# Kernel optimization log

Hardware: AMD Instinct MI355X
Metric: run time of the kernel (lower is better)

The kernel has to match this reference:

```python
import jax, jax.numpy as jnp
import numpy as np

B, R, F, H, DIM = 256, 64, 2048, 512, 512

def setup_inputs() -> dict:
    key = jax.random.key(0)
    ks = jax.random.split(key, 8)
    s = lambda n: 1.0 / np.sqrt(n)
    return {
        "features": jax.random.normal(ks[0], (B, R, F), jnp.float32),
        "prev": jax.random.normal(ks[1], (B, H), jnp.float32),
        "W_w": jax.random.normal(ks[2], (F, DIM), jnp.float32) * s(F),
        "W_b": jnp.zeros((DIM,), jnp.float32),
        "W2_w": jax.random.normal(ks[3], (H, DIM), jnp.float32) * s(H),
        "W2_b": jnp.zeros((DIM,), jnp.float32),
        "W3_w": jax.random.normal(ks[4], (DIM, 1), jnp.float32) * s(DIM),
        "W3_b": jnp.zeros((1,), jnp.float32),
    }

def reference(features, prev, W_w, W_b, W2_w, W2_b, W3_w, W3_b):
    # prev: [B,H] -> [B,1,DIM]
    p = (prev @ W2_w + W2_b)[:, None, :]
    # features: [B,R,F] -> [B,R,DIM]
    c = jnp.einsum('brf,fd->brd', features, W_w) + W_b
    c = jnp.tanh(c + p)
    score = jnp.einsum('brd,do->bro', c, W3_w) + W3_b  # [B,R,1]
    aw = jax.nn.softmax(score, axis=1)
    q = jnp.sum(aw * features, axis=1)  # [B,F]
    return q
```

## Files before the change

kernel.cpp:

```cpp
#include <hip/hip_runtime.h>
#include <hip/hip_bf16.h>


#define B_ 256
#define R_ 64
#define F_ 2048
#define H_ 512
#define DIM_ 512

typedef short bf16x8 __attribute__((ext_vector_type(8)));
typedef float f32x4 __attribute__((ext_vector_type(4)));

__device__ __forceinline__ ushort f2bf(float x) {
  __hip_bfloat16 h = __float2bfloat16(x);
  return __builtin_bit_cast(ushort, h);
}

__device__ __forceinline__ uint2 pack4(float4 x) {
  uint2 r;
  r.x = (uint)f2bf(x.x) | ((uint)f2bf(x.y) << 16);
  r.y = (uint)f2bf(x.z) | ((uint)f2bf(x.w) << 16);
  return r;
}

__global__ __launch_bounds__(256) void setup_k(const float* __restrict__ Ww,
                                               ushort* __restrict__ wpack,
                                               const float* __restrict__ prev,
                                               const float* __restrict__ W2w,
                                               const float* __restrict__ W2b,
                                               const float* __restrict__ Wb,
                                               float* __restrict__ pprime) {
  __shared__ float lprev[8][H_];
  if (blockIdx.x < 4096) {
    int idx = blockIdx.x * 256 + threadIdx.x;
    float v = Ww[idx];
    int k = idx >> 9;
    int d = idx & 511;
    int kt = k >> 5, kr = k & 31;
    int g = kr >> 3, i = kr & 7;
    int ctg = d >> 4, c = d & 15;
    size_t dst = ((size_t)((kt * 32 + ctg) * 64 + g * 16 + c)) * 8 + (size_t)i;
    wpack[dst] = f2bf(v);
    return;
  }
  int pb = blockIdx.x - 4096;
  int bg = pb >> 3;
  int d0 = (pb & 7) * 64;
  int t = threadIdx.x;
  const float4* src = reinterpret_cast<const float4*>(prev + (size_t)bg * 8 * H_);
  float4* dst = reinterpret_cast<float4*>(&lprev[0][0]);
  for (int i = t; i < 8 * H_ / 4; i += 256) dst[i] = src[i];
  __syncthreads();
  int d = d0 + (t & 63);
  int bq = t >> 6;
  float a0 = 0.f, a1 = 0.f;
  #pragma unroll 8
  for (int h = 0; h < H_; ++h) {
    float wv = W2w[h * DIM_ + d];
    a0 += lprev[bq][h] * wv;
    a1 += lprev[bq + 4][h] * wv;
  }
  float bias = W2b[d] + Wb[d];
  pprime[(size_t)(bg * 8 + bq) * DIM_ + d] = a0 + bias;
  pprime[(size_t)(bg * 8 + bq + 4) * DIM_ + d] = a1 + bias;
}

__device__ __forceinline__ float fast_tanh(float x) {
  float e = __expf(2.f * x);
  return 1.f - 2.f / (e + 1.f);
}

__global__ __launch_bounds__(512, 4) void score_k(const float* __restrict__ feat,
                                                  const ushort* __restrict__ wpack,
                                                  const float* __restrict__ pprime,
                                                  const float* __restrict__ W3,
                                                  float* __restrict__ sp) {
  int slice = blockIdx.x >> 8;
  int b = blockIdx.x & 255;
  int t = threadIdx.x;
  int wid = t >> 6;
  int l = t & 63;
  int l15 = l & 15, g = l >> 4;
  const float* featB = feat + (size_t)b * R_ * F_;

  __shared__ uint4 frg[2][512];
  __shared__ float lds_part[8][R_];

  f32x4 acc[4][2];
  #pragma unroll
  for (int rt = 0; rt < 4; ++rt)
    #pragma unroll
    for (int ct = 0; ct < 2; ++ct)
      acc[rt][ct] = (f32x4){0.f, 0.f, 0.f, 0.f};

  int r0 = t >> 4;
  int c4 = t & 15;
  const float* ga0 = featB + (size_t)r0 * F_ + (size_t)(c4 * 4);
  const float* ga1 = featB + (size_t)(r0 + 32) * F_ + (size_t)(c4 * 4);
  int kcw = c4 >> 1, half = c4 & 1;
  int wi0 = kcw * 64 + (r0 ^ kcw);
  int wi1 = kcw * 64 + ((r0 + 32) ^ kcw);

  const ushort* wp = wpack + (size_t)(slice * 16 + wid * 2) * 512 + (size_t)l * 8;

#define LOADB(dst, kt) do {                                          \
    const ushort* wpk_ = wp + (size_t)(kt) * 32768;                  \
    dst[0][0] = *reinterpret_cast<const uint4*>(wpk_);               \
    dst[0][1] = *reinterpret_cast<const uint4*>(wpk_ + 512);         \
    dst[1][0] = *reinterpret_cast<const uint4*>(wpk_ + 16384);       \
    dst[1][1] = *reinterpret_cast<const uint4*>(wpk_ + 16384 + 512); \
  } while (0)

#define CVTW(fb, ASET) do {                                          \
    uint2* d0_ = reinterpret_cast<uint2*>(&frg[fb][wi0]);            \
    d0_[half] = pack4(ASET[0]);                                      \
    uint2* d1_ = reinterpret_cast<uint2*>(&frg[fb][wi1]);            \
    d1_[half] = pack4(ASET[1]);                                      \
  } while (0)

#define MFMA8(AF, BSET, s_) do {                                     \
    _Pragma("unroll")                                                \
    for (int ct_ = 0; ct_ < 2; ++ct_) {                              \
      bf16x8 bv_ = __builtin_bit_cast(bf16x8, BSET[s_][ct_]);        \
      _Pragma("unroll")                                              \
      for (int rt_ = 0; rt_ < 4; ++rt_)                              \
        acc[rt_][ct_] = __builtin_amdgcn_mfma_f32_16x16x32_bf16(     \
            __builtin_bit_cast(bf16x8, AF[rt_]), bv_, acc[rt_][ct_], 0, 0, 0); \
    }                                                                \
  } while (0)

#define FENCE() asm volatile("" ::: "memory")
#define BAR() do { FENCE(); __builtin_amdgcn_s_barrier(); FENCE(); } while (0)
#define LGKM0() do {                                                 \
    asm volatile("s_waitcnt lgkmcnt(0)" ::: "memory");               \
    __builtin_amdgcn_sched_barrier(0);                               \
  } while (0)

#define REGION(kt, aCvt, aFill, bUse, bFill) do {                    \
    uint4 af0_[4], af1_[4];                                          \
    _Pragma("unroll")                                                \
    for (int rt_ = 0; rt_ < 4; ++rt_)                                \
      af0_[rt_] = frg[(kt) & 1][g * 64 + ((rt_ * 16 + l15) ^ g)];    \
    if ((kt) < 30) {                                                 \
      aFill[0] = *reinterpret_cast<const float4*>(ga0 + ((kt) + 2) * 64); \
      aFill[1] = *reinterpret_cast<const float4*>(ga1 + ((kt) + 2) * 64); \
    }                                                                \
    if ((kt) < 31) LOADB(bFill, (kt) + 1);                           \
    BAR();                                                           \
    LGKM0();                                                         \
    __builtin_amdgcn_s_setprio(1);                                   \
    MFMA8(af0_, bUse, 0);                                            \
    __builtin_amdgcn_s_setprio(0);                                   \
    BAR();                                                           \
    _Pragma("unroll")                                                \
    for (int rt_ = 0; rt_ < 4; ++rt_) {                              \
      int kc_ = 4 + g;                                               \
      af1_[rt_] = frg[(kt) & 1][kc_ * 64 + ((rt_ * 16 + l15) ^ kc_)]; \
    }                                                                \
    if ((kt) < 31) CVTW(((kt) + 1) & 1, aCvt);                       \
    BAR();                                                           \
    LGKM0();                                                         \
    __builtin_amdgcn_s_setprio(1);                                   \
    MFMA8(af1_, bUse, 1);                                            \
    __builtin_amdgcn_s_setprio(0);                                   \
    BAR();                                                           \
  } while (0)

  float4 aS0[2], aS1[2];
  uint4 b0[2][2], b1[2][2];

  aS0[0] = *reinterpret_cast<const float4*>(ga0);
  aS0[1] = *reinterpret_cast<const float4*>(ga1);
  LOADB(b0, 0);
  CVTW(0, aS0);
  aS1[0] = *reinterpret_cast<const float4*>(ga0 + 64);
  aS1[1] = *reinterpret_cast<const float4*>(ga1 + 64);
  LGKM0();
  BAR();

  for (int kt = 0; kt < 32; kt += 2) {
    REGION(kt, aS1, aS0, b0, b1);
    REGION(kt + 1, aS0, aS1, b1, b0);
  }

#undef LOADB
#undef CVTW
#undef MFMA8
#undef REGION
#undef BAR
#undef LGKM0
#undef FENCE

  float pp[2], w3v[2];
  #pragma unroll
  for (int ct = 0; ct < 2; ++ct) {
    int col = slice * 256 + wid * 32 + ct * 16 + l15;
    pp[ct] = pprime[b * DIM_ + col];
    w3v[ct] = W3[col];
  }
  #pragma unroll
  for (int rt = 0; rt < 4; ++rt) {
    #pragma unroll
    for (int j = 0; j < 4; ++j) {
      float v = fast_tanh(acc[rt][0][j] + pp[0]) * w3v[0]
              + fast_tanh(acc[rt][1][j] + pp[1]) * w3v[1];
      v += __shfl_xor(v, 1);
      v += __shfl_xor(v, 2);
      v += __shfl_xor(v, 4);
      v += __shfl_xor(v, 8);
      if (l15 == 0) lds_part[wid][rt * 16 + g * 4 + j] = v;
    }
  }
  __syncthreads();

  if (t < R_) {
    float s = 0.f;
    #pragma unroll
    for (int w = 0; w < 8; ++w) s += lds_part[w][t];
    sp[((size_t)b * 2 + slice) * R_ + t] = s;
  }
}

__global__ __launch_bounds__(256) void wsum_k(const float* __restrict__ feat,
                                              const float* __restrict__ sp,
                                              float* __restrict__ out) {
  int b = blockIdx.x >> 2;
  int f0 = (blockIdx.x & 3) * 512;
  int t = threadIdx.x;
  __shared__ float lds_aw[R_];

  if (t < R_) {
    float s = sp[((size_t)b * 2 + 0) * R_ + t] + sp[((size_t)b * 2 + 1) * R_ + t];
    float m = s;
    #pragma unroll
    for (int off = 32; off >= 1; off >>= 1) m = fmaxf(m, __shfl_xor(m, off));
    float e = __expf(s - m);
    float su = e;
    #pragma unroll
    for (int off = 32; off >= 1; off >>= 1) su += __shfl_xor(su, off);
    lds_aw[t] = e / su;
  }
  __syncthreads();

  const float* fp = feat + (size_t)b * R_ * F_ + f0 + t * 2;
  float qx = 0.f, qy = 0.f;
  #pragma unroll 8
  for (int r = 0; r < R_; ++r) {
    float a = lds_aw[r];
    float2 v = *reinterpret_cast<const float2*>(fp + (size_t)r * F_);
    qx += a * v.x;
    qy += a * v.y;
  }
  *reinterpret_cast<float2*>(out + (size_t)b * F_ + f0 + t * 2) = (float2){qx, qy};
}

extern "C" void kernel_launch(void* const* d_in, const int* in_sizes, int n_in,
                              void* d_out, int out_size, void* d_ws, size_t ws_size,
                              hipStream_t stream) {
  const float* feat = (const float*)d_in[0];
  const float* prev = (const float*)d_in[1];
  const float* Ww   = (const float*)d_in[2];
  const float* Wb   = (const float*)d_in[3];
  const float* W2w  = (const float*)d_in[4];
  const float* W2b  = (const float*)d_in[5];
  const float* W3w  = (const float*)d_in[6];
  float* out = (float*)d_out;

  ushort* wpack  = (ushort*)d_ws;
  float*  pprime = (float*)((char*)d_ws + (size_t)F_ * DIM_ * 2);
  float*  sp     = (float*)((char*)d_ws + (size_t)F_ * DIM_ * 2
                                        + (size_t)B_ * DIM_ * 4);

  setup_k<<<4096 + 256, 256, 0, stream>>>(Ww, wpack, prev, W2w, W2b, Wb, pprime);
  score_k<<<B_ * 2, 512, 0, stream>>>(feat, wpack, pprime, W3w, sp);
  wsum_k<<<B_ * 4, 256, 0, stream>>>(feat, sp, out);
}
```

Measured before the change: 117.7 us.

## Split score kernel into single-wave blocks over 64-column DIM slices

Restructures the score kernel so each 64-thread block handles one batch and 64 DIM columns. Each wave loads and converts the full feature tile itself, with no block barriers and a single LDS buffer. Partial scores for 8 slices are summed in the softmax kernel. This removes barrier synchronisation and raises block count. In exchange, each batch's features are read and converted to bf16 eight times instead of twice, and register pressure is higher.

After: 199.7 us. 69.7% more time.

```diff
diff --git a/kernel.cpp b/kernel.cpp
--- a/kernel.cpp
+++ b/kernel.cpp
@@ -70,131 +70,112 @@
   return 1.f - 2.f / (e + 1.f);
 }
 
-__global__ __launch_bounds__(512, 4) void score_k(const float* __restrict__ feat,
-                                                  const ushort* __restrict__ wpack,
-                                                  const float* __restrict__ pprime,
-                                                  const float* __restrict__ W3,
-                                                  float* __restrict__ sp) {
+__global__ __launch_bounds__(64, 2) void score_k(const float* __restrict__ feat,
+                                                 const ushort* __restrict__ wpack,
+                                                 const float* __restrict__ pprime,
+                                                 const float* __restrict__ W3,
+                                                 float* __restrict__ sp) {
   int slice = blockIdx.x >> 8;
   int b = blockIdx.x & 255;
-  int t = threadIdx.x;
-  int wid = t >> 6;
-  int l = t & 63;
+  int l = threadIdx.x;
   int l15 = l & 15, g = l >> 4;
   const float* featB = feat + (size_t)b * R_ * F_;
 
-  __shared__ uint4 frg[2][512];
-  __shared__ float lds_part[8][R_];
-
-  f32x4 acc[4][2];
+  __shared__ uint4 frg[512];
+  __shared__ float sc[R_];
+
+  f32x4 acc[4][4];
   #pragma unroll
   for (int rt = 0; rt < 4; ++rt)
     #pragma unroll
-    for (int ct = 0; ct < 2; ++ct)
+    for (int ct = 0; ct < 4; ++ct)
       acc[rt][ct] = (f32x4){0.f, 0.f, 0.f, 0.f};
 
-  int r0 = t >> 4;
-  int c4 = t & 15;
-  const float* ga0 = featB + (size_t)r0 * F_ + (size_t)(c4 * 4);
-  const float* ga1 = featB + (size_t)(r0 + 32) * F_ + (size_t)(c4 * 4);
+  int c4 = l & 15, r4 = l >> 4;
   int kcw = c4 >> 1, half = c4 & 1;
-  int wi0 = kcw * 64 + (r0 ^ kcw);
-  int wi1 = kcw * 64 + ((r0 + 32) ^ kcw);
-
-  const ushort* wp = wpack + (size_t)(slice * 16 + wid * 2) * 512 + (size_t)l * 8;
+  const float* aptr = featB + (size_t)r4 * F_ + (size_t)(c4 * 4);
+  float4 rA[16];
+
+  const ushort* wp = wpack + (size_t)(slice * 4) * 512 + (size_t)l * 8;
+
+#define LOADA(kt) do {                                               \
+    _Pragma("unroll")                                                \
+    for (int j_ = 0; j_ < 16; ++j_)                                  \
+      rA[j_] = *reinterpret_cast<const float4*>(                     \
+          aptr + (size_t)(j_ * 4) * F_ + (size_t)(kt) * 64);         \
+  } while (0)
+
+#define CVTW() do {                                                  \
+    _Pragma("unroll")                                                \
+    for (int j_ = 0; j_ < 16; ++j_) {                                \
+      int row_ = r4 + 4 * j_;                                        \
+      uint2* d_ = reinterpret_cast<uint2*>(&frg[kcw * 64 + (row_ ^ kcw)]); \
+      d_[half] = pack4(rA[j_]);                                      \
+    }                                                                \
+  } while (0)
 
 #define LOADB(dst, kt) do {                                          \
     const ushort* wpk_ = wp + (size_t)(kt) * 32768;                  \
-    dst[0][0] = *reinterpret_cast<const uint4*>(wpk_);               \
-    dst[0][1] = *reinterpret_cast<const uint4*>(wpk_ + 512);         \
-    dst[1][0] = *reinterpret_cast<const uint4*>(wpk_ + 16384);       \
-    dst[1][1] = *reinterpret_cast<const uint4*>(wpk_ + 16384 + 512); \
-  } while (0)
-
-#define CVTW(fb, ASET) do {                                          \
-    uint2* d0_ = reinterpret_cast<uint2*>(&frg[fb][wi0]);            \
-    d0_[half] = pack4(ASET[0]);                                      \
-    uint2* d1_ = reinterpret_cast<uint2*>(&frg[fb][wi1]);            \
-    d1_[half] = pack4(ASET[1]);                                      \
-  } while (0)
-
-#define MFMA8(AF, BSET, s_) do {                                     \
-    _Pragma("unroll")                                                \
-    for (int ct_ = 0; ct_ < 2; ++ct_) {                              \
-      bf16x8 bv_ = __builtin_bit_cast(bf16x8, BSET[s_][ct_]);        \
+    _Pragma("unroll")                                                \
+    for (int s_ = 0; s_ < 2; ++s_)                                   \
+      _Pragma("unroll")                                              \
+      for (int ct_ = 0; ct_ < 4; ++ct_)                              \
+        dst[s_ * 4 + ct_] = *reinterpret_cast<const uint4*>(         \
+            wpk_ + s_ * 16384 + ct_ * 512);                          \
+  } while (0)
+
+#define STEP(k, BUSE, BNXT) do {                                     \
+    if ((k) < 31) LOADB(BNXT, (k) + 1);                              \
+    uint4 af0_[4], af1_[4];                                          \
+    _Pragma("unroll")                                                \
+    for (int rt_ = 0; rt_ < 4; ++rt_)                                \
+      af0_[rt_] = frg[g * 64 + ((rt_ * 16 + l15) ^ g)];              \
+    _Pragma("unroll")                                                \
+    for (int rt_ = 0; rt_ < 4; ++rt_) {                              \
+      int kc_ = 4 + g;                                               \
+      af1_[rt_] = frg[kc_ * 64 + ((rt_ * 16 + l15) ^ kc_)];          \
+    }                                                                \
+    if ((k) < 31) CVTW();             \
+    if ((k) < 30) LOADA((k) + 2);                                    \
+    _Pragma("unroll")                                                \
+    for (int ct_ = 0; ct_ < 4; ++ct_) {                              \
+      bf16x8 bv_ = __builtin_bit_cast(bf16x8, BUSE[ct_]);            \
       _Pragma("unroll")                                              \
       for (int rt_ = 0; rt_ < 4; ++rt_)                              \
         acc[rt_][ct_] = __builtin_amdgcn_mfma_f32_16x16x32_bf16(     \
-            __builtin_bit_cast(bf16x8, AF[rt_]), bv_, acc[rt_][ct_], 0, 0, 0); \
-    }                                                                \
-  } while (0)
-
-#define FENCE() asm volatile("" ::: "memory")
-#define BAR() do { FENCE(); __builtin_amdgcn_s_barrier(); FENCE(); } while (0)
-#define LGKM0() do {                                                 \
-    asm volatile("s_waitcnt lgkmcnt(0)" ::: "memory");               \
-    __builtin_amdgcn_sched_barrier(0);                               \
-  } while (0)
-
-#define REGION(kt, aCvt, aFill, bUse, bFill) do {                    \
-    uint4 af0_[4], af1_[4];                                          \
-    _Pragma("unroll")                                                \
-    for (int rt_ = 0; rt_ < 4; ++rt_)                                \
-      af0_[rt_] = frg[(kt) & 1][g * 64 + ((rt_ * 16 + l15) ^ g)];    \
-    if ((kt) < 30) {                                                 \
-      aFill[0] = *reinterpret_cast<const float4*>(ga0 + ((kt) + 2) * 64); \
-      aFill[1] = *reinterpret_cast<const float4*>(ga1 + ((kt) + 2) * 64); \
-    }                                                                \
-    if ((kt) < 31) LOADB(bFill, (kt) + 1);                           \
-    BAR();                                                           \
-    LGKM0();                                                         \
-    __builtin_amdgcn_s_setprio(1);                                   \
-    MFMA8(af0_, bUse, 0);                                            \
-    __builtin_amdgcn_s_setprio(0);                                   \
-    BAR();                                                           \
-    _Pragma("unroll")                                                \
-    for (int rt_ = 0; rt_ < 4; ++rt_) {                              \
-      int kc_ = 4 + g;                                               \
-      af1_[rt_] = frg[(kt) & 1][kc_ * 64 + ((rt_ * 16 + l15) ^ kc_)]; \
-    }                                                                \
-    if ((kt) < 31) CVTW(((kt) + 1) & 1, aCvt);                       \
-    BAR();                                                           \
-    LGKM0();                                                         \
-    __builtin_amdgcn_s_setprio(1);                                   \
-    MFMA8(af1_, bUse, 1);                                            \
-    __builtin_amdgcn_s_setprio(0);                                   \
-    BAR();                                                           \
-  } while (0)
-
-  float4 aS0[2], aS1[2];
-  uint4 b0[2][2], b1[2][2];
-
-  aS0[0] = *reinterpret_cast<const float4*>(ga0);
-  aS0[1] = *reinterpret_cast<const float4*>(ga1);
-  LOADB(b0, 0);
-  CVTW(0, aS0);
-  aS1[0] = *reinterpret_cast<const float4*>(ga0 + 64);
-  aS1[1] = *reinterpret_cast<const float4*>(ga1 + 64);
-  LGKM0();
-  BAR();
-
-  for (int kt = 0; kt < 32; kt += 2) {
-    REGION(kt, aS1, aS0, b0, b1);
-    REGION(kt + 1, aS0, aS1, b1, b0);
-  }
-
+            __builtin_bit_cast(bf16x8, af0_[rt_]), bv_, acc[rt_][ct_], 0, 0, 0); \
+    }                                                                \
+    _Pragma("unroll")                                                \
+    for (int ct_ = 0; ct_ < 4; ++ct_) {                              \
+      bf16x8 bv_ = __builtin_bit_cast(bf16x8, BUSE[4 + ct_]);        \
+      _Pragma("unroll")                                              \
+      for (int rt_ = 0; rt_ < 4; ++rt_)                              \
+        acc[rt_][ct_] = __builtin_amdgcn_mfma_f32_16x16x32_bf16(     \
+            __builtin_bit_cast(bf16x8, af1_[rt_]), bv_, acc[rt_][ct_], 0, 0, 0); \
+    }                                                                \
+  } while (0)
+
+  uint4 bE[8], bO[8];
+  LOADA(0);
+  LOADB(bE, 0);
+  CVTW();
+  LOADA(1);
+
+  #pragma unroll 1
+  for (int k = 0; k < 32; k += 2) {
+    STEP(k, bE, bO);
+    STEP(k + 1, bO, bE);
+  }
+
+#undef LOADA
+#undef CVTW
 #undef LOADB
-#undef CVTW
-#undef MFMA8
-#undef REGION
-#undef BAR
-#undef LGKM0
-#undef FENCE
-
-  float pp[2], w3v[2];
+#undef STEP
+
+  float pp[4], w3v[4];
   #pragma unroll
-  for (int ct = 0; ct < 2; ++ct) {
-    int col = slice * 256 + wid * 32 + ct * 16 + l15;
+  for (int ct = 0; ct < 4; ++ct) {
+    int col = slice * 64 + ct * 16 + l15;
     pp[ct] = pprime[b * DIM_ + col];
     w3v[ct] = W3[col];
   }
@@ -203,22 +184,17 @@
     #pragma unroll
     for (int j = 0; j < 4; ++j) {
       float v = fast_tanh(acc[rt][0][j] + pp[0]) * w3v[0]
-              + fast_tanh(acc[rt][1][j] + pp[1]) * w3v[1];
+              + fast_tanh(acc[rt][1][j] + pp[1]) * w3v[1]
+              + fast_tanh(acc[rt][2][j] + pp[2]) * w3v[2]
+              + fast_tanh(acc[rt][3][j] + pp[3]) * w3v[3];
       v += __shfl_xor(v, 1);
       v += __shfl_xor(v, 2);
       v += __shfl_xor(v, 4);
       v += __shfl_xor(v, 8);
-      if (l15 == 0) lds_part[wid][rt * 16 + g * 4 + j] = v;
+      if (l15 == 0) sc[rt * 16 + g * 4 + j] = v;
     }
   }
-  __syncthreads();
-
-  if (t < R_) {
-    float s = 0.f;
-    #pragma unroll
-    for (int w = 0; w < 8; ++w) s += lds_part[w][t];
-    sp[((size_t)b * 2 + slice) * R_ + t] = s;
-  }
+  sp[((size_t)b * 8 + slice) * R_ + l] = sc[l];
 }
 
 __global__ __launch_bounds__(256) void wsum_k(const float* __restrict__ feat,
@@ -230,7 +206,9 @@
   __shared__ float lds_aw[R_];
 
   if (t < R_) {
-    float s = sp[((size_t)b * 2 + 0) * R_ + t] + sp[((size_t)b * 2 + 1) * R_ + t];
+    float s = 0.f;
+    #pragma unroll
+    for (int i = 0; i < 8; ++i) s += sp[((size_t)b * 8 + i) * R_ + t];
     float m = s;
     #pragma unroll
     for (int off = 32; off >= 1; off >>= 1) m = fmaxf(m, __shfl_xor(m, off));
@@ -272,6 +250,6 @@
                                         + (size_t)B_ * DIM_ * 4);
 
   setup_k<<<4096 + 256, 256, 0, stream>>>(Ww, wpack, prev, W2w, W2b, Wb, pprime);
-  score_k<<<B_ * 2, 512, 0, stream>>>(feat, wpack, pprime, W3w, sp);
+  score_k<<<B_ * 8, 64, 0, stream>>>(feat, wpack, pprime, W3w, sp);
   wsum_k<<<B_ * 4, 256, 0, stream>>>(feat, sp, out);
 }
```
